# Performance work log

Measured on AMD Instinct MI355X. Metric: run time of the kernel, lower is better.

## Reference

```python
import jax, jax.numpy as jnp
import numpy as np

N_NODES = 50000
N_EDGES = 800000
D_IN = 16
H = 128
D_OUT = 8
N_LAYERS = 4


def _init_linear(key, fan_in, fan_out):
    # torch init: weight ~ N(0, 1/sqrt(in_features)), bias = 0
    W = jax.random.normal(key, (fan_in, fan_out), dtype=jnp.float32) / jnp.sqrt(jnp.float32(fan_in))
    b = jnp.zeros((fan_out,), dtype=jnp.float32)
    return W, b


def _mlp2(x, W1, b1, W2, b2):
    # 2-layer MLP: Linear -> GELU(exact) -> Linear
    h = jax.nn.gelu(x @ W1 + b1, approximate=False)
    return h @ W2 + b2


def setup_inputs() -> dict:
    key = jax.random.key(0)
    ks = jax.random.split(key, 16)
    node_features = jax.random.normal(ks[0], (N_NODES, D_IN), dtype=jnp.float32)
    edge_index = jax.random.randint(ks[1], (2, N_EDGES), 0, N_NODES, dtype=jnp.int64 if jax.config.jax_enable_x64 else jnp.int32)
    enc_W1, enc_b1 = _init_linear(ks[2], D_IN, H)
    enc_W2, enc_b2 = _init_linear(ks[3], H, H)
    dec_W1, dec_b1 = _init_linear(ks[4], H, H)
    dec_W2, dec_b2 = _init_linear(ks[5], H, D_OUT)
    # stacked per-layer params for the message-passing blocks
    eW1 = jnp.stack([_init_linear(jax.random.fold_in(ks[6], l), 2 * H, H)[0] for l in range(N_LAYERS)])
    eW2 = jnp.stack([_init_linear(jax.random.fold_in(ks[7], l), H, H)[0] for l in range(N_LAYERS)])
    nW1 = jnp.stack([_init_linear(jax.random.fold_in(ks[8], l), 2 * H, H)[0] for l in range(N_LAYERS)])
    nW2 = jnp.stack([_init_linear(jax.random.fold_in(ks[9], l), H, H)[0] for l in range(N_LAYERS)])
    eb1 = jnp.zeros((N_LAYERS, H), dtype=jnp.float32)
    eb2 = jnp.zeros((N_LAYERS, H), dtype=jnp.float32)
    nb1 = jnp.zeros((N_LAYERS, H), dtype=jnp.float32)
    nb2 = jnp.zeros((N_LAYERS, H), dtype=jnp.float32)
    return dict(node_features=node_features, edge_index=edge_index,
                enc_W1=enc_W1, enc_b1=enc_b1, enc_W2=enc_W2, enc_b2=enc_b2,
                edge_W1=eW1, edge_b1=eb1, edge_W2=eW2, edge_b2=eb2,
                node_W1=nW1, node_b1=nb1, node_W2=nW2, node_b2=nb2,
                dec_W1=dec_W1, dec_b1=dec_b1, dec_W2=dec_W2, dec_b2=dec_b2)


def reference(node_features, edge_index,
              enc_W1, enc_b1, enc_W2, enc_b2,
              edge_W1, edge_b1, edge_W2, edge_b2,
              node_W1, node_b1, node_W2, node_b2,
              dec_W1, dec_b1, dec_W2, dec_b2):
    src = edge_index[0]
    dst = edge_index[1]
    # encode
    h = _mlp2(node_features, enc_W1, enc_b1, enc_W2, enc_b2)  # [N, H]
    # process: residual message-passing blocks with sum aggregation
    for l in range(edge_W1.shape[0]):
        edge_input = jnp.concatenate([h[src], h[dst]], axis=-1)  # [E, 2H]
        message = _mlp2(edge_input, edge_W1[l], edge_b1[l], edge_W2[l], edge_b2[l])  # [E, H]
        aggregated = jax.ops.segment_sum(message, dst, num_segments=h.shape[0])  # [N, H]
        node_update = _mlp2(jnp.concatenate([h, aggregated], axis=-1),
                            node_W1[l], node_b1[l], node_W2[l], node_b2[l])
        h = h + node_update
    # decode
    return _mlp2(h, dec_W1, dec_b1, dec_W2, dec_b2)  # [N, D_OUT]
```

## Files before the change

kernel.cpp:

```cpp
#include <hip/hip_runtime.h>
#include <math.h>


constexpr int H = 128;
constexpr int NTHR = 256;
constexpr int TE = 64;
constexpr int TILE = 32;

using bf16x8 = __attribute__((ext_vector_type(8))) short;
using f32x4  = __attribute__((ext_vector_type(4))) float;

__device__ __forceinline__ float gelu_fast(float x) {
    const float u = fabsf(x) * 0.70710678118654752440f;
    const float t = __builtin_amdgcn_rcpf(fmaf(0.3275911f, u, 1.f));
    float p = fmaf(1.061405429f, t, -1.453152027f);
    p = fmaf(p, t, 1.421413741f);
    p = fmaf(p, t, -0.284496736f);
    p = fmaf(p, t, 0.254829592f);
    p = p * t;
    const float e = __expf(-u * u);
    float er = fmaf(-p, e, 1.f);
    er = copysignf(er, x);
    return 0.5f * x * (1.f + er);
}

__device__ __forceinline__ unsigned short f2bf(float f) {
    unsigned int u = __builtin_bit_cast(unsigned int, f);
    u = (u + 0x7fffu + ((u >> 16) & 1u)) >> 16;
    return (unsigned short)u;
}

__device__ __forceinline__ float bf2f_lo(unsigned int v) {
    return __builtin_bit_cast(float, v << 16);
}
__device__ __forceinline__ float bf2f_hi(unsigned int v) {
    return __builtin_bit_cast(float, v & 0xffff0000u);
}

__global__ __launch_bounds__(NTHR) void wcvt_kernel(
    const float* __restrict__ W, unsigned short* __restrict__ Wt,
    int K, int Ncols, int total) {
    const int i = blockIdx.x * NTHR + threadIdx.x;
    if (i >= total) return;
    const int per = K * Ncols;
    const int l = i / per;
    const int r = i - l * per;
    const int n = r % Ncols;
    const int k = r / Ncols;
    Wt[(size_t)l * per + n * K + k] = f2bf(W[i]);
}

__global__ __launch_bounds__(NTHR) void wcvt_top_kernel(
    const float* __restrict__ W, unsigned short* __restrict__ Wt, int total) {
    const int i = blockIdx.x * NTHR + threadIdx.x;
    if (i >= total) return;
    const int per = H * H;
    const int l = i / per;
    const int r = i - l * per;
    const int k = r / H;
    const int o = r % H;
    Wt[(size_t)l * H * 2 * H + o * 2 * H + k] =
        f2bf(W[(size_t)l * 2 * H * H + k * H + o]);
}

__global__ __launch_bounds__(H) void wcomb_kernel(
    const float* __restrict__ eW2, const float* __restrict__ eb2,
    const float* __restrict__ nW1, unsigned short* __restrict__ W1tc,
    float* __restrict__ cvec) {
    const int l = blockIdx.y;
    const int j = blockIdx.x;
    const int o = threadIdx.x;
    const float* w1 = nW1 + (size_t)l * 2 * H * H + (size_t)H * H;
    const float* row = (j < H) ? (eW2 + (size_t)l * H * H + (size_t)j * H)
                               : (eb2 + (size_t)l * H);
    float s = 0.f;
#pragma unroll 4
    for (int c = 0; c < H; ++c) s = fmaf(row[c], w1[(size_t)c * H + o], s);
    if (j < H)
        W1tc[(size_t)l * H * 2 * H + o * 2 * H + H + j] = f2bf(s);
    else
        cvec[(size_t)l * H + o] = s;
}

__global__ __launch_bounds__(NTHR) void deg_kernel(const int* __restrict__ dst,
                                                   int* __restrict__ deg, int E) {
    const int e = blockIdx.x * NTHR + threadIdx.x;
    if (e < E) atomicAdd(&deg[dst[e]], 1);
}

__global__ __launch_bounds__(1024) void scan1_kernel(
    const int* __restrict__ deg, int* __restrict__ out,
    int* __restrict__ bsum, int N) {
    __shared__ int buf[1024];
    const int t = threadIdx.x;
    const int i = blockIdx.x * 1024 + t;
    const int x = (i < N) ? deg[i] : 0;
    buf[t] = x;
    __syncthreads();
    int v = x;
    for (int off = 1; off < 1024; off <<= 1) {
        const int y = (t >= off) ? buf[t - off] : 0;
        __syncthreads();
        v += y;
        buf[t] = v;
        __syncthreads();
    }
    if (i < N) out[i] = v - x;
    if (t == 1023) bsum[blockIdx.x] = v;
}

__global__ void scan2_kernel(int* __restrict__ bsum, int nb) {
    if (threadIdx.x == 0) {
        int acc = 0;
        for (int i = 0; i < nb; ++i) {
            const int t = bsum[i];
            bsum[i] = acc;
            acc += t;
        }
    }
}

__global__ __launch_bounds__(NTHR) void scan3_kernel(
    int* __restrict__ out, int* __restrict__ cursor,
    const int* __restrict__ bsum, int N, int E) {
    const int i = blockIdx.x * NTHR + threadIdx.x;
    if (i < N) {
        const int v = out[i] + bsum[i >> 10];
        out[i] = v;
        cursor[i] = v;
    } else if (i == N) {
        out[N] = E;
    }
}

__global__ __launch_bounds__(NTHR) void chunk_kernel(
    const int* __restrict__ rowStart, int* __restrict__ chunkLo, int N) {
    const int n = blockIdx.x * NTHR + threadIdx.x;
    if (n < N) atomicMin(&chunkLo[rowStart[n] >> 5], n);
}

__global__ __launch_bounds__(NTHR) void scatter_kernel(
    const int* __restrict__ src, const int* __restrict__ dst,
    int* __restrict__ cursor, int* __restrict__ srcS, int E) {
    const int e = blockIdx.x * NTHR + threadIdx.x;
    if (e >= E) return;
    const int pos = atomicAdd(&cursor[dst[e]], 1);
    srcS[pos] = src[e];
}

__global__ __launch_bounds__(NTHR) void ab_kernel(
    const unsigned short* __restrict__ h_bf,
    const unsigned short* __restrict__ W1t,
    const float* __restrict__ b1, unsigned short* __restrict__ A,
    float* __restrict__ Bout, int N) {
    __shared__ __align__(16) unsigned short X[TE * H];
    const int t = threadIdx.x;
    const int lane = t & 63;
    const int w = t >> 6;
    const int n0 = blockIdx.x * TE;
    const int l15 = lane & 15;
    const int lq = lane >> 4;

#pragma unroll
    for (int i = 0; i < 4; ++i) {
        const int c = i * NTHR + t;
        const int row = c >> 4;
        const int col8 = c & 15;
        const int n = n0 + row;
        const int4 v = (n < N)
            ? *reinterpret_cast<const int4*>(h_bf + (size_t)n * H + col8 * 8)
            : make_int4(0, 0, 0, 0);
        const int byteoff = row * 256 + ((col8 * 16) ^ ((row & 7) << 4));
        *reinterpret_cast<int4*>(reinterpret_cast<char*>(X) + byteoff) = v;
    }

    const int half = w >> 1;
    const int cbase = (w & 1) * 64;
    bf16x8 Bf[4][4];
#pragma unroll
    for (int cg = 0; cg < 4; ++cg) {
        const int col = cbase + cg * 16 + l15;
#pragma unroll
        for (int s = 0; s < 4; ++s)
            Bf[cg][s] = *reinterpret_cast<const bf16x8*>(
                W1t + (size_t)col * 256 + half * 128 + s * 32 + lq * 8);
    }
    __syncthreads();

    f32x4 acc[4][4];
#pragma unroll
    for (int rg = 0; rg < 4; ++rg)
#pragma unroll
        for (int cg = 0; cg < 4; ++cg) acc[rg][cg] = (f32x4)0.f;

#pragma unroll
    for (int s = 0; s < 4; ++s) {
        bf16x8 a[4];
#pragma unroll
        for (int rg = 0; rg < 4; ++rg) {
            const int row = rg * 16 + l15;
            const int byteoff = row * 256 + ((s * 64 + lq * 16) ^ ((row & 7) << 4));
            a[rg] = *reinterpret_cast<const bf16x8*>(
                reinterpret_cast<const char*>(X) + byteoff);
        }
#pragma unroll
        for (int rg = 0; rg < 4; ++rg)
#pragma unroll
            for (int cg = 0; cg < 4; ++cg)
                acc[rg][cg] = __builtin_amdgcn_mfma_f32_16x16x32_bf16(
                    a[rg], Bf[cg][s], acc[rg][cg], 0, 0, 0);
    }

#pragma unroll
    for (int cg = 0; cg < 4; ++cg) {
        const int col = cbase + cg * 16 + l15;
        const float bb = (half == 1) ? b1[col] : 0.f;
#pragma unroll
        for (int rg = 0; rg < 4; ++rg) {
#pragma unroll
            for (int r = 0; r < 4; ++r) {
                const int row = rg * 16 + lq * 4 + r;
                const int n = n0 + row;
                if (n < N) {
                    if (half == 0)
                        A[(size_t)n * H + col] = f2bf(acc[rg][cg][r]);
                    else
                        Bout[(size_t)n * H + col] = acc[rg][cg][r] + bb;
                }
            }
        }
    }
}

__global__ __launch_bounds__(NTHR) void edge_gather_kernel(
    const unsigned short* __restrict__ A, const float* __restrict__ B,
    const int* __restrict__ srcS, const int* __restrict__ rowStart,
    const int* __restrict__ chunkLo, float* __restrict__ aggG, int N, int E) {
    const int lane = threadIdx.x & 63;
    const int c = blockIdx.x * 4 + (threadIdx.x >> 6);
    const int nWaves = (E >> 5) + 1;
    if (c >= nWaves) return;
    int n = chunkLo[c];
    if (n >= N) return;
    const int Wend = (c + 1) * 32;
    const int c2 = lane * 2;
    int r0 = rowStart[n];
    while (true) {
        const int r1 = rowStart[n + 1];
        const float2 bv = *reinterpret_cast<const float2*>(B + (size_t)n * H + c2);
        float s0 = 0.f, s1 = 0.f;
        int e = r0;
        for (; e + 4 <= r1; e += 4) {
            const int sa = srcS[e];
            const int sb = srcS[e + 1];
            const int sc = srcS[e + 2];
            const int sd = srcS[e + 3];
            const unsigned int va =
                *reinterpret_cast<const unsigned int*>(A + (size_t)sa * H + c2);
            const unsigned int vb =
                *reinterpret_cast<const unsigned int*>(A + (size_t)sb * H + c2);
            const unsigned int vc =
                *reinterpret_cast<const unsigned int*>(A + (size_t)sc * H + c2);
            const unsigned int vd =
                *reinterpret_cast<const unsigned int*>(A + (size_t)sd * H + c2);
            s0 += gelu_fast(bf2f_lo(va) + bv.x);
            s1 += gelu_fast(bf2f_hi(va) + bv.y);
            s0 += gelu_fast(bf2f_lo(vb) + bv.x);
            s1 += gelu_fast(bf2f_hi(vb) + bv.y);
            s0 += gelu_fast(bf2f_lo(vc) + bv.x);
            s1 += gelu_fast(bf2f_hi(vc) + bv.y);
            s0 += gelu_fast(bf2f_lo(vd) + bv.x);
            s1 += gelu_fast(bf2f_hi(vd) + bv.y);
        }
        for (; e < r1; ++e) {
            const int s = srcS[e];
            const unsigned int av =
                *reinterpret_cast<const unsigned int*>(A + (size_t)s * H + c2);
            s0 += gelu_fast(bf2f_lo(av) + bv.x);
            s1 += gelu_fast(bf2f_hi(av) + bv.y);
        }
        *reinterpret_cast<float2*>(aggG + (size_t)n * H + c2) =
            make_float2(s0, s1);
        if (++n >= N) break;
        r0 = r1;
        if (r0 >= Wend) break;
    }
}

template <bool PROD>
__global__ __launch_bounds__(NTHR) void node_fused_kernel(
    float* __restrict__ h, unsigned short* __restrict__ h_bf,
    const float* __restrict__ aggG, const int* __restrict__ deg,
    const unsigned short* __restrict__ W1tc, const float* __restrict__ b1,
    const float* __restrict__ cvec, const unsigned short* __restrict__ W2t,
    const float* __restrict__ b2, const unsigned short* __restrict__ eW1tN,
    const float* __restrict__ eb1N, unsigned short* __restrict__ A_out,
    float* __restrict__ B_out, int N) {
    __shared__ __align__(16) unsigned short X[TE * 256];
    __shared__ int degS[TE];
    const int t = threadIdx.x;
    const int lane = t & 63;
    const int w = t >> 6;
    const int n0 = blockIdx.x * TE;
    const int l15 = lane & 15;
    const int lq = lane >> 4;

    if (t < TE) degS[t] = (n0 + t < N) ? deg[n0 + t] : 0;
#pragma unroll
    for (int i = 0; i < 8; ++i) {
        const int c = i * NTHR + t;
        const int row = c >> 5;
        const int col8 = c & 31;
        const int n = n0 + row;
        int4 v = make_int4(0, 0, 0, 0);
        if (n < N) {
            if (col8 < 16) {
                v = *reinterpret_cast<const int4*>(h_bf + (size_t)n * H + col8 * 8);
            } else {
                const float* ap = aggG + (size_t)n * H + (col8 - 16) * 8;
                union { int4 q; unsigned short us[8]; } u;
#pragma unroll
                for (int j = 0; j < 8; ++j) u.us[j] = f2bf(ap[j]);
                v = u.q;
            }
        }
        const int byteoff = row * 512 + ((col8 * 16) ^ ((row & 7) << 4));
        *reinterpret_cast<int4*>(reinterpret_cast<char*>(X) + byteoff) = v;
    }

    bf16x8 B1[2][8];
#pragma unroll
    for (int cg = 0; cg < 2; ++cg) {
        const int col = w * 32 + cg * 16 + l15;
#pragma unroll
        for (int s = 0; s < 8; ++s)
            B1[cg][s] = *reinterpret_cast<const bf16x8*>(
                W1tc + (size_t)col * 256 + s * 32 + lq * 8);
    }
    __syncthreads();

    f32x4 acc[4][2];
#pragma unroll
    for (int rg = 0; rg < 4; ++rg)
#pragma unroll
        for (int cg = 0; cg < 2; ++cg) acc[rg][cg] = (f32x4)0.f;

#pragma unroll
    for (int s = 0; s < 8; ++s) {
        bf16x8 a[4];
#pragma unroll
        for (int rg = 0; rg < 4; ++rg) {
            const int row = rg * 16 + l15;
            const int byteoff = row * 512 + ((s * 64 + lq * 16) ^ ((row & 7) << 4));
            a[rg] = *reinterpret_cast<const bf16x8*>(
                reinterpret_cast<const char*>(X) + byteoff);
        }
#pragma unroll
        for (int rg = 0; rg < 4; ++rg)
#pragma unroll
            for (int cg = 0; cg < 2; ++cg)
                acc[rg][cg] = __builtin_amdgcn_mfma_f32_16x16x32_bf16(
                    a[rg], B1[cg][s], acc[rg][cg], 0, 0, 0);
    }
    __syncthreads();

#pragma unroll
    for (int cg = 0; cg < 2; ++cg) {
        const int col = w * 32 + cg * 16 + l15;
        const float bb = b1[col];
        const float cc = cvec[col];
#pragma unroll
        for (int rg = 0; rg < 4; ++rg) {
#pragma unroll
            for (int r = 0; r < 4; ++r) {
                const int row = rg * 16 + lq * 4 + r;
                const float v =
                    gelu_fast(acc[rg][cg][r] + bb + (float)degS[row] * cc);
                const int byteoff = row * 256 + ((col * 2) ^ ((row & 7) << 4));
                *reinterpret_cast<unsigned short*>(
                    reinterpret_cast<char*>(X) + byteoff) = f2bf(v);
            }
        }
    }

    bf16x8 B2[2][4];
#pragma unroll
    for (int cg = 0; cg < 2; ++cg) {
        const int col = w * 32 + cg * 16 + l15;
#pragma unroll
        for (int s = 0; s < 4; ++s)
            B2[cg][s] = *reinterpret_cast<const bf16x8*>(
                W2t + (size_t)col * 128 + s * 32 + lq * 8);
    }
    __syncthreads();

    f32x4 acc2[4][2];
#pragma unroll
    for (int rg = 0; rg < 4; ++rg)
#pragma unroll
        for (int cg = 0; cg < 2; ++cg) acc2[rg][cg] = (f32x4)0.f;

#pragma unroll
    for (int s = 0; s < 4; ++s) {
        bf16x8 a[4];
#pragma unroll
        for (int rg = 0; rg < 4; ++rg) {
            const int row = rg * 16 + l15;
            const int byteoff = row * 256 + ((s * 64 + lq * 16) ^ ((row & 7) << 4));
            a[rg] = *reinterpret_cast<const bf16x8*>(
                reinterpret_cast<const char*>(X) + byteoff);
        }
#pragma unroll
        for (int rg = 0; rg < 4; ++rg)
#pragma unroll
            for (int cg = 0; cg < 2; ++cg)
                acc2[rg][cg] = __builtin_amdgcn_mfma_f32_16x16x32_bf16(
                    a[rg], B2[cg][s], acc2[rg][cg], 0, 0, 0);
    }

#pragma unroll
    for (int cg = 0; cg < 2; ++cg) {
        const int col = w * 32 + cg * 16 + l15;
        const float bb = b2[col];
#pragma unroll
        for (int rg = 0; rg < 4; ++rg) {
#pragma unroll
            for (int r = 0; r < 4; ++r) {
                const int row = rg * 16 + lq * 4 + r;
                const int n = n0 + row;
                if (n < N) {
                    const float hv = h[(size_t)n * H + col] + acc2[rg][cg][r] + bb;
                    h[(size_t)n * H + col] = hv;
                    const unsigned short hb = f2bf(hv);
                    h_bf[(size_t)n * H + col] = hb;
                    if (PROD) {
                        const int byteoff =
                            16384 + row * 256 + ((col * 2) ^ ((row & 7) << 4));
                        *reinterpret_cast<unsigned short*>(
                            reinterpret_cast<char*>(X) + byteoff) = hb;
                    }
                } else if (PROD) {
                    const int byteoff =
                        16384 + row * 256 + ((col * 2) ^ ((row & 7) << 4));
                    *reinterpret_cast<unsigned short*>(
                        reinterpret_cast<char*>(X) + byteoff) = 0;
                }
            }
        }
    }

    if (PROD) {
        bf16x8 B3[2][4], B4[2][4];
#pragma unroll
        for (int cg = 0; cg < 2; ++cg) {
            const int col = w * 32 + cg * 16 + l15;
#pragma unroll
            for (int s = 0; s < 4; ++s) {
                B3[cg][s] = *reinterpret_cast<const bf16x8*>(
                    eW1tN + (size_t)col * 256 + s * 32 + lq * 8);
                B4[cg][s] = *reinterpret_cast<const bf16x8*>(
                    eW1tN + (size_t)col * 256 + 128 + s * 32 + lq * 8);
            }
        }
        __syncthreads();

        f32x4 acc3[4][2], acc4[4][2];
#pragma unroll
        for (int rg = 0; rg < 4; ++rg)
#pragma unroll
            for (int cg = 0; cg < 2; ++cg) {
                acc3[rg][cg] = (f32x4)0.f;
                acc4[rg][cg] = (f32x4)0.f;
            }

#pragma unroll
        for (int s = 0; s < 4; ++s) {
            bf16x8 a[4];
#pragma unroll
            for (int rg = 0; rg < 4; ++rg) {
                const int row = rg * 16 + l15;
                const int byteoff =
                    16384 + row * 256 + ((s * 64 + lq * 16) ^ ((row & 7) << 4));
                a[rg] = *reinterpret_cast<const bf16x8*>(
                    reinterpret_cast<const char*>(X) + byteoff);
            }
#pragma unroll
            for (int rg = 0; rg < 4; ++rg)
#pragma unroll
                for (int cg = 0; cg < 2; ++cg) {
                    acc3[rg][cg] = __builtin_amdgcn_mfma_f32_16x16x32_bf16(
                        a[rg], B3[cg][s], acc3[rg][cg], 0, 0, 0);
                    acc4[rg][cg] = __builtin_amdgcn_mfma_f32_16x16x32_bf16(
                        a[rg], B4[cg][s], acc4[rg][cg], 0, 0, 0);
                }
        }

#pragma unroll
        for (int cg = 0; cg < 2; ++cg) {
            const int col = w * 32 + cg * 16 + l15;
            const float bb = eb1N[col];
#pragma unroll
            for (int rg = 0; rg < 4; ++rg) {
#pragma unroll
                for (int r = 0; r < 4; ++r) {
                    const int row = rg * 16 + lq * 4 + r;
                    const int n = n0 + row;
                    if (n < N) {
                        A_out[(size_t)n * H + col] = f2bf(acc3[rg][cg][r]);
                        B_out[(size_t)n * H + col] = acc4[rg][cg][r] + bb;
                    }
                }
            }
        }
    }
}

template <int K4>
__device__ __forceinline__ void mlp_layer(const float* __restrict__ W,
                                          const float* lds, int ldsStride,
                                          int c0, int egBase,
                                          float a0[8], float a1[8]) {
#pragma unroll 2
    for (int k4 = 0; k4 < K4; ++k4) {
        const float w00 = W[(k4 * 4 + 0) * H + c0];
        const float w01 = W[(k4 * 4 + 1) * H + c0];
        const float w02 = W[(k4 * 4 + 2) * H + c0];
        const float w03 = W[(k4 * 4 + 3) * H + c0];
        const float w10 = W[(k4 * 4 + 0) * H + c0 + 64];
        const float w11 = W[(k4 * 4 + 1) * H + c0 + 64];
        const float w12 = W[(k4 * 4 + 2) * H + c0 + 64];
        const float w13 = W[(k4 * 4 + 3) * H + c0 + 64];
#pragma unroll
        for (int e = 0; e < 8; ++e) {
            const float4 x = *reinterpret_cast<const float4*>(
                &lds[(egBase + e) * ldsStride + k4 * 4]);
            a0[e] = fmaf(x.x, w00, a0[e]);
            a0[e] = fmaf(x.y, w01, a0[e]);
            a0[e] = fmaf(x.z, w02, a0[e]);
            a0[e] = fmaf(x.w, w03, a0[e]);
            a1[e] = fmaf(x.x, w10, a1[e]);
            a1[e] = fmaf(x.y, w11, a1[e]);
            a1[e] = fmaf(x.z, w12, a1[e]);
            a1[e] = fmaf(x.w, w13, a1[e]);
        }
    }
}

__global__ __launch_bounds__(NTHR) void encode_kernel(
    const float* __restrict__ nf, const float* __restrict__ W1,
    const float* __restrict__ b1, const float* __restrict__ W2,
    const float* __restrict__ b2, float* __restrict__ h,
    unsigned short* __restrict__ h_bf, int N) {
    __shared__ float xin[TILE * 16];
    __shared__ float hm[TILE * H];
    const int t = threadIdx.x;
    const int n0 = blockIdx.x * TILE;
    const int c0 = t & 63;
    const int eg = t >> 6;

    for (int i = t; i < TILE * 16; i += NTHR) {
        const int gi = n0 * 16 + i;
        xin[i] = (gi < N * 16) ? nf[gi] : 0.f;
    }
    __syncthreads();

    float a0[8], a1[8];
#pragma unroll
    for (int e = 0; e < 8; ++e) { a0[e] = 0.f; a1[e] = 0.f; }
    mlp_layer<4>(W1, xin, 16, c0, eg * 8, a0, a1);
    {
        const float bb0 = b1[c0], bb1 = b1[c0 + 64];
#pragma unroll
        for (int e = 0; e < 8; ++e) {
            hm[(eg * 8 + e) * H + c0] = gelu_fast(a0[e] + bb0);
            hm[(eg * 8 + e) * H + c0 + 64] = gelu_fast(a1[e] + bb1);
        }
    }
    __syncthreads();
#pragma unroll
    for (int e = 0; e < 8; ++e) { a0[e] = 0.f; a1[e] = 0.f; }
    mlp_layer<32>(W2, hm, H, c0, eg * 8, a0, a1);
    const float bb0 = b2[c0], bb1 = b2[c0 + 64];
#pragma unroll
    for (int e = 0; e < 8; ++e) {
        const int n = n0 + eg * 8 + e;
        if (n < N) {
            const float v0 = a0[e] + bb0, v1 = a1[e] + bb1;
            h[(size_t)n * H + c0] = v0;
            h[(size_t)n * H + c0 + 64] = v1;
            h_bf[(size_t)n * H + c0] = f2bf(v0);
            h_bf[(size_t)n * H + c0 + 64] = f2bf(v1);
        }
    }
}

__global__ __launch_bounds__(NTHR) void decode_kernel(
    const float* __restrict__ h, const float* __restrict__ W1,
    const float* __restrict__ b1, const float* __restrict__ W2,
    const float* __restrict__ b2, float* __restrict__ out, int N) {
    __shared__ float xin[TILE * H];
    __shared__ float hm[TILE * 132];
    const int t = threadIdx.x;
    const int n0 = blockIdx.x * TILE;
    const int c0 = t & 63;
    const int eg = t >> 6;
    {
        const int col = t & 127;
        for (int e = t >> 7; e < TILE; e += 2) {
            const int n = n0 + e;
            xin[e * H + col] = (n < N) ? h[(size_t)n * H + col] : 0.f;
        }
    }
    __syncthreads();

    float a0[8], a1[8];
#pragma unroll
    for (int e = 0; e < 8; ++e) { a0[e] = 0.f; a1[e] = 0.f; }
    mlp_layer<32>(W1, xin, H, c0, eg * 8, a0, a1);
    {
        const float bb0 = b1[c0], bb1 = b1[c0 + 64];
#pragma unroll
        for (int e = 0; e < 8; ++e) {
            hm[(eg * 8 + e) * 132 + c0] = gelu_fast(a0[e] + bb0);
            hm[(eg * 8 + e) * 132 + c0 + 64] = gelu_fast(a1[e] + bb1);
        }
    }
    __syncthreads();
    {
        const int e = t >> 3;
        const int o = t & 7;
        const int n = n0 + e;
        float acc = b2[o];
#pragma unroll 4
        for (int k = 0; k < H; ++k)
            acc = fmaf(hm[e * 132 + k], W2[k * 8 + o], acc);
        if (n < N) out[n * 8 + o] = acc;
    }
}

extern "C" void kernel_launch(void* const* d_in, const int* in_sizes, int n_in,
                              void* d_out, int out_size, void* d_ws,
                              size_t ws_size, hipStream_t stream) {
    (void)n_in; (void)out_size; (void)ws_size;
    const float* nf      = (const float*)d_in[0];
    const int*   ei      = (const int*)d_in[1];
    const float* enc_W1  = (const float*)d_in[2];
    const float* enc_b1  = (const float*)d_in[3];
    const float* enc_W2  = (const float*)d_in[4];
    const float* enc_b2  = (const float*)d_in[5];
    const float* edge_W1 = (const float*)d_in[6];
    const float* edge_b1 = (const float*)d_in[7];
    const float* edge_W2 = (const float*)d_in[8];
    const float* edge_b2 = (const float*)d_in[9];
    const float* node_W1 = (const float*)d_in[10];
    const float* node_b1 = (const float*)d_in[11];
    const float* node_W2 = (const float*)d_in[12];
    const float* node_b2 = (const float*)d_in[13];
    const float* dec_W1  = (const float*)d_in[14];
    const float* dec_b1  = (const float*)d_in[15];
    const float* dec_W2  = (const float*)d_in[16];
    const float* dec_b2  = (const float*)d_in[17];

    const int N = in_sizes[0] / 16;
    const int E = in_sizes[1] / 2;
    const int L = in_sizes[7] / H;
    const int numChunks = (E >> 5) + 1;

    char* ws = (char*)d_ws;
    float* h    = (float*)ws;                    ws += (size_t)N * H * 4;
    float* aggG = (float*)ws;                    ws += (size_t)N * H * 4;
    float* Bf32 = (float*)ws;                    ws += (size_t)N * H * 4;
    unsigned short* h_bf  = (unsigned short*)ws; ws += (size_t)N * H * 2;
    unsigned short* A_bf  = (unsigned short*)ws; ws += (size_t)N * H * 2;
    int* srcS     = (int*)ws;                    ws += (size_t)E * 4;
    int* deg      = (int*)ws;                    ws += (size_t)N * 4;
    int* rowStart = (int*)ws;                    ws += (size_t)(N + 1) * 4;
    int* cursor   = (int*)ws;                    ws += (size_t)N * 4;
    int* bsum     = (int*)ws;                    ws += (size_t)256 * 4;
    int* chunkLo  = (int*)ws;                    ws += (size_t)numChunks * 4;
    unsigned short* eW1t = (unsigned short*)ws;  ws += (size_t)L * 2 * H * H * 2;
    unsigned short* nW1tc = (unsigned short*)ws; ws += (size_t)L * 2 * H * H * 2;
    unsigned short* nW2t = (unsigned short*)ws;  ws += (size_t)L * H * H * 2;
    float* cvec   = (float*)ws;                  ws += (size_t)L * H * 4;

    const int* srcArr = ei;
    const int* dstArr = ei + E;

    {
        const int t1 = L * 2 * H * H, t2 = L * H * H;
        wcvt_kernel<<<(t1 + NTHR - 1) / NTHR, NTHR, 0, stream>>>(edge_W1, eW1t, 2 * H, H, t1);
        wcvt_kernel<<<(t2 + NTHR - 1) / NTHR, NTHR, 0, stream>>>(node_W2, nW2t, H, H, t2);
        wcvt_top_kernel<<<(t2 + NTHR - 1) / NTHR, NTHR, 0, stream>>>(node_W1, nW1tc, t2);
        wcomb_kernel<<<dim3(H + 1, L), H, 0, stream>>>(edge_W2, edge_b2,
                                                       node_W1, nW1tc, cvec);
    }

    hipMemsetAsync(deg, 0, (size_t)N * 4, stream);
    deg_kernel<<<(E + NTHR - 1) / NTHR, NTHR, 0, stream>>>(dstArr, deg, E);
    const int nScanB = (N + 1023) / 1024;
    scan1_kernel<<<nScanB, 1024, 0, stream>>>(deg, rowStart, bsum, N);
    scan2_kernel<<<1, 64, 0, stream>>>(bsum, nScanB);
    scan3_kernel<<<(N + 1 + NTHR - 1) / NTHR, NTHR, 0, stream>>>(
        rowStart, cursor, bsum, N, E);
    hipMemsetAsync(chunkLo, 0x7f, (size_t)numChunks * 4, stream);
    chunk_kernel<<<(N + NTHR - 1) / NTHR, NTHR, 0, stream>>>(rowStart, chunkLo, N);
    scatter_kernel<<<(E + NTHR - 1) / NTHR, NTHR, 0, stream>>>(srcArr, dstArr,
                                                               cursor, srcS, E);

    const int encBlocks  = (N + TILE - 1) / TILE;
    const int tileBlocks = (N + TE - 1) / TE;
    const int gatherBlks = (numChunks + 3) / 4;

    encode_kernel<<<encBlocks, NTHR, 0, stream>>>(nf, enc_W1, enc_b1, enc_W2,
                                                  enc_b2, h, h_bf, N);
    ab_kernel<<<tileBlocks, NTHR, 0, stream>>>(h_bf, eW1t, edge_b1, A_bf, Bf32,
                                               N);
    for (int l = 0; l < L; ++l) {
        edge_gather_kernel<<<gatherBlks, NTHR, 0, stream>>>(
            A_bf, Bf32, srcS, rowStart, chunkLo, aggG, N, E);
        if (l + 1 < L) {
            node_fused_kernel<true><<<tileBlocks, NTHR, 0, stream>>>(
                h, h_bf, aggG, deg, nW1tc + (size_t)l * 2 * H * H,
                node_b1 + (size_t)l * H, cvec + (size_t)l * H,
                nW2t + (size_t)l * H * H, node_b2 + (size_t)l * H,
                eW1t + (size_t)(l + 1) * 2 * H * H,
                edge_b1 + (size_t)(l + 1) * H, A_bf, Bf32, N);
        } else {
            node_fused_kernel<false><<<tileBlocks, NTHR, 0, stream>>>(
                h, h_bf, aggG, deg, nW1tc + (size_t)l * 2 * H * H,
                node_b1 + (size_t)l * H, cvec + (size_t)l * H,
                nW2t + (size_t)l * H * H, node_b2 + (size_t)l * H, nullptr,
                nullptr, nullptr, nullptr, N);
        }
    }
    decode_kernel<<<encBlocks, NTHR, 0, stream>>>(h, dec_W1, dec_b1, dec_W2,
                                                  dec_b2, (float*)d_out, N);
}
```

Measured before the change: 719.0 us.

## Fuse edge gather-aggregation into node kernel with double-buffered A/B

Moves the per-destination edge gather, GELU and sum directly into the node MLP kernel. Each wave aggregates 16 node rows and writes the bf16 result straight into shared memory, which removes the separate gather kernel, the fp32 aggregation buffer round-trip, and the chunk-map setup. A and B are double-buffered so the next layer's projections can be written while the current ones are still being read. Source indices are pre-scaled by 256 bytes to simplify addressing, and the three weight-conversion kernels are merged into one launch. The cost is that per-tile gather work is now uneven, with a full tile of row aggregation serialized across only 4 waves before the MFMA work begins.

```diff
diff --git a/kernel.cpp b/kernel.cpp
--- a/kernel.cpp
+++ b/kernel.cpp
@@ -37,30 +37,37 @@
     return __builtin_bit_cast(float, v & 0xffff0000u);
 }
 
-__global__ __launch_bounds__(NTHR) void wcvt_kernel(
-    const float* __restrict__ W, unsigned short* __restrict__ Wt,
-    int K, int Ncols, int total) {
+__global__ __launch_bounds__(NTHR) void prep_kernel(
+    const float* __restrict__ eW1, const float* __restrict__ nW2,
+    const float* __restrict__ nW1, unsigned short* __restrict__ eW1t,
+    unsigned short* __restrict__ nW2t, unsigned short* __restrict__ nW1tc,
+    int t1, int t2) {
     const int i = blockIdx.x * NTHR + threadIdx.x;
-    if (i >= total) return;
-    const int per = K * Ncols;
-    const int l = i / per;
-    const int r = i - l * per;
-    const int n = r % Ncols;
-    const int k = r / Ncols;
-    Wt[(size_t)l * per + n * K + k] = f2bf(W[i]);
-}
-
-__global__ __launch_bounds__(NTHR) void wcvt_top_kernel(
-    const float* __restrict__ W, unsigned short* __restrict__ Wt, int total) {
-    const int i = blockIdx.x * NTHR + threadIdx.x;
-    if (i >= total) return;
-    const int per = H * H;
-    const int l = i / per;
-    const int r = i - l * per;
-    const int k = r / H;
-    const int o = r % H;
-    Wt[(size_t)l * H * 2 * H + o * 2 * H + k] =
-        f2bf(W[(size_t)l * 2 * H * H + k * H + o]);
+    if (i < t1) {
+        const int per = 2 * H * H;
+        const int l = i / per;
+        const int r = i - l * per;
+        const int n = r % H;
+        const int k = r / H;
+        eW1t[(size_t)l * per + n * 2 * H + k] = f2bf(eW1[i]);
+    } else if (i < t1 + t2) {
+        const int j = i - t1;
+        const int per = H * H;
+        const int l = j / per;
+        const int r = j - l * per;
+        const int n = r % H;
+        const int k = r / H;
+        nW2t[(size_t)l * per + n * H + k] = f2bf(nW2[j]);
+    } else if (i < t1 + 2 * t2) {
+        const int j = i - t1 - t2;
+        const int per = H * H;
+        const int l = j / per;
+        const int r = j - l * per;
+        const int k = r / H;
+        const int o = r % H;
+        nW1tc[(size_t)l * H * 2 * H + o * 2 * H + k] =
+            f2bf(nW1[(size_t)l * 2 * H * H + k * H + o]);
+    }
 }
 
 __global__ __launch_bounds__(H) void wcomb_kernel(
@@ -133,19 +140,13 @@
     }
 }
 
-__global__ __launch_bounds__(NTHR) void chunk_kernel(
-    const int* __restrict__ rowStart, int* __restrict__ chunkLo, int N) {
-    const int n = blockIdx.x * NTHR + threadIdx.x;
-    if (n < N) atomicMin(&chunkLo[rowStart[n] >> 5], n);
-}
-
 __global__ __launch_bounds__(NTHR) void scatter_kernel(
     const int* __restrict__ src, const int* __restrict__ dst,
     int* __restrict__ cursor, int* __restrict__ srcS, int E) {
     const int e = blockIdx.x * NTHR + threadIdx.x;
     if (e >= E) return;
     const int pos = atomicAdd(&cursor[dst[e]], 1);
-    srcS[pos] = src[e];
+    srcS[pos] = src[e] << 8;
 }
 
 __global__ __launch_bounds__(NTHR) void ab_kernel(
@@ -232,70 +233,16 @@
     }
 }
 
-__global__ __launch_bounds__(NTHR) void edge_gather_kernel(
-    const unsigned short* __restrict__ A, const float* __restrict__ B,
-    const int* __restrict__ srcS, const int* __restrict__ rowStart,
-    const int* __restrict__ chunkLo, float* __restrict__ aggG, int N, int E) {
-    const int lane = threadIdx.x & 63;
-    const int c = blockIdx.x * 4 + (threadIdx.x >> 6);
-    const int nWaves = (E >> 5) + 1;
-    if (c >= nWaves) return;
-    int n = chunkLo[c];
-    if (n >= N) return;
-    const int Wend = (c + 1) * 32;
-    const int c2 = lane * 2;
-    int r0 = rowStart[n];
-    while (true) {
-        const int r1 = rowStart[n + 1];
-        const float2 bv = *reinterpret_cast<const float2*>(B + (size_t)n * H + c2);
-        float s0 = 0.f, s1 = 0.f;
-        int e = r0;
-        for (; e + 4 <= r1; e += 4) {
-            const int sa = srcS[e];
-            const int sb = srcS[e + 1];
-            const int sc = srcS[e + 2];
-            const int sd = srcS[e + 3];
-            const unsigned int va =
-                *reinterpret_cast<const unsigned int*>(A + (size_t)sa * H + c2);
-            const unsigned int vb =
-                *reinterpret_cast<const unsigned int*>(A + (size_t)sb * H + c2);
-            const unsigned int vc =
-                *reinterpret_cast<const unsigned int*>(A + (size_t)sc * H + c2);
-            const unsigned int vd =
-                *reinterpret_cast<const unsigned int*>(A + (size_t)sd * H + c2);
-            s0 += gelu_fast(bf2f_lo(va) + bv.x);
-            s1 += gelu_fast(bf2f_hi(va) + bv.y);
-            s0 += gelu_fast(bf2f_lo(vb) + bv.x);
-            s1 += gelu_fast(bf2f_hi(vb) + bv.y);
-            s0 += gelu_fast(bf2f_lo(vc) + bv.x);
-            s1 += gelu_fast(bf2f_hi(vc) + bv.y);
-            s0 += gelu_fast(bf2f_lo(vd) + bv.x);
-            s1 += gelu_fast(bf2f_hi(vd) + bv.y);
-        }
-        for (; e < r1; ++e) {
-            const int s = srcS[e];
-            const unsigned int av =
-                *reinterpret_cast<const unsigned int*>(A + (size_t)s * H + c2);
-            s0 += gelu_fast(bf2f_lo(av) + bv.x);
-            s1 += gelu_fast(bf2f_hi(av) + bv.y);
-        }
-        *reinterpret_cast<float2*>(aggG + (size_t)n * H + c2) =
-            make_float2(s0, s1);
-        if (++n >= N) break;
-        r0 = r1;
-        if (r0 >= Wend) break;
-    }
-}
-
 template <bool PROD>
 __global__ __launch_bounds__(NTHR) void node_fused_kernel(
     float* __restrict__ h, unsigned short* __restrict__ h_bf,
-    const float* __restrict__ aggG, const int* __restrict__ deg,
-    const unsigned short* __restrict__ W1tc, const float* __restrict__ b1,
-    const float* __restrict__ cvec, const unsigned short* __restrict__ W2t,
-    const float* __restrict__ b2, const unsigned short* __restrict__ eW1tN,
-    const float* __restrict__ eb1N, unsigned short* __restrict__ A_out,
-    float* __restrict__ B_out, int N) {
+    const unsigned short* __restrict__ A_g, const float* __restrict__ B_g,
+    const int* __restrict__ srcS, const int* __restrict__ rowStart,
+    const int* __restrict__ deg, const unsigned short* __restrict__ W1tc,
+    const float* __restrict__ b1, const float* __restrict__ cvec,
+    const unsigned short* __restrict__ W2t, const float* __restrict__ b2,
+    const unsigned short* __restrict__ eW1tN, const float* __restrict__ eb1N,
+    unsigned short* __restrict__ A_out, float* __restrict__ B_out, int N) {
     __shared__ __align__(16) unsigned short X[TE * 256];
     __shared__ int degS[TE];
     const int t = threadIdx.x;
@@ -306,26 +253,68 @@
     const int lq = lane >> 4;
 
     if (t < TE) degS[t] = (n0 + t < N) ? deg[n0 + t] : 0;
-#pragma unroll
-    for (int i = 0; i < 8; ++i) {
+
+#pragma unroll
+    for (int i = 0; i < 4; ++i) {
         const int c = i * NTHR + t;
-        const int row = c >> 5;
-        const int col8 = c & 31;
+        const int row = c >> 4;
+        const int col8 = c & 15;
         const int n = n0 + row;
-        int4 v = make_int4(0, 0, 0, 0);
-        if (n < N) {
-            if (col8 < 16) {
-                v = *reinterpret_cast<const int4*>(h_bf + (size_t)n * H + col8 * 8);
-            } else {
-                const float* ap = aggG + (size_t)n * H + (col8 - 16) * 8;
-                union { int4 q; unsigned short us[8]; } u;
-#pragma unroll
-                for (int j = 0; j < 8; ++j) u.us[j] = f2bf(ap[j]);
-                v = u.q;
-            }
-        }
+        const int4 v = (n < N)
+            ? *reinterpret_cast<const int4*>(h_bf + (size_t)n * H + col8 * 8)
+            : make_int4(0, 0, 0, 0);
         const int byteoff = row * 512 + ((col8 * 16) ^ ((row & 7) << 4));
         *reinterpret_cast<int4*>(reinterpret_cast<char*>(X) + byteoff) = v;
+    }
+
+    {
+        const char* Abase = (const char*)A_g + (size_t)(lane * 4);
+        const int c2 = lane * 2;
+        for (int rr = 0; rr < 16; ++rr) {
+            const int row = w * 16 + rr;
+            const int n = n0 + row;
+            float s0 = 0.f, s1 = 0.f;
+            if (n < N) {
+                const int r0 = rowStart[n];
+                const int r1 = rowStart[n + 1];
+                const float2 bv =
+                    *reinterpret_cast<const float2*>(B_g + (size_t)n * H + c2);
+                int e = r0;
+                for (; e + 4 <= r1; e += 4) {
+                    const int sa = srcS[e];
+                    const int sb = srcS[e + 1];
+                    const int sc = srcS[e + 2];
+                    const int sd = srcS[e + 3];
+                    const unsigned int va =
+                        *reinterpret_cast<const unsigned int*>(Abase + sa);
+                    const unsigned int vb =
+                        *reinterpret_cast<const unsigned int*>(Abase + sb);
+                    const unsigned int vc =
+                        *reinterpret_cast<const unsigned int*>(Abase + sc);
+                    const unsigned int vd =
+                        *reinterpret_cast<const unsigned int*>(Abase + sd);
+                    s0 += gelu_fast(bf2f_lo(va) + bv.x);
+                    s1 += gelu_fast(bf2f_hi(va) + bv.y);
+                    s0 += gelu_fast(bf2f_lo(vb) + bv.x);
+                    s1 += gelu_fast(bf2f_hi(vb) + bv.y);
+                    s0 += gelu_fast(bf2f_lo(vc) + bv.x);
+                    s1 += gelu_fast(bf2f_hi(vc) + bv.y);
+                    s0 += gelu_fast(bf2f_lo(vd) + bv.x);
+                    s1 += gelu_fast(bf2f_hi(vd) + bv.y);
+                }
+                for (; e < r1; ++e) {
+                    const unsigned int av =
+                        *reinterpret_cast<const unsigned int*>(Abase + srcS[e]);
+                    s0 += gelu_fast(bf2f_lo(av) + bv.x);
+                    s1 += gelu_fast(bf2f_hi(av) + bv.y);
+                }
+            }
+            const unsigned int packed =
+                (unsigned int)f2bf(s0) | ((unsigned int)f2bf(s1) << 16);
+            const int byteoff = row * 512 + ((256 + lane * 4) ^ ((row & 7) << 4));
+            *reinterpret_cast<unsigned int*>(reinterpret_cast<char*>(X) +
+                                             byteoff) = packed;
+        }
     }
 
     bf16x8 B1[2][8];
@@ -664,20 +653,21 @@
     const int N = in_sizes[0] / 16;
     const int E = in_sizes[1] / 2;
     const int L = in_sizes[7] / H;
-    const int numChunks = (E >> 5) + 1;
 
     char* ws = (char*)d_ws;
     float* h    = (float*)ws;                    ws += (size_t)N * H * 4;
-    float* aggG = (float*)ws;                    ws += (size_t)N * H * 4;
-    float* Bf32 = (float*)ws;                    ws += (size_t)N * H * 4;
-    unsigned short* h_bf  = (unsigned short*)ws; ws += (size_t)N * H * 2;
-    unsigned short* A_bf  = (unsigned short*)ws; ws += (size_t)N * H * 2;
+    float* Bbuf[2];
+    Bbuf[0] = (float*)ws;                        ws += (size_t)N * H * 4;
+    Bbuf[1] = (float*)ws;                        ws += (size_t)N * H * 4;
+    unsigned short* h_bf = (unsigned short*)ws;  ws += (size_t)N * H * 2;
+    unsigned short* Abuf[2];
+    Abuf[0] = (unsigned short*)ws;               ws += (size_t)N * H * 2;
+    Abuf[1] = (unsigned short*)ws;               ws += (size_t)N * H * 2;
     int* srcS     = (int*)ws;                    ws += (size_t)E * 4;
     int* deg      = (int*)ws;                    ws += (size_t)N * 4;
     int* rowStart = (int*)ws;                    ws += (size_t)(N + 1) * 4;
     int* cursor   = (int*)ws;                    ws += (size_t)N * 4;
     int* bsum     = (int*)ws;                    ws += (size_t)256 * 4;
-    int* chunkLo  = (int*)ws;                    ws += (size_t)numChunks * 4;
     unsigned short* eW1t = (unsigned short*)ws;  ws += (size_t)L * 2 * H * H * 2;
     unsigned short* nW1tc = (unsigned short*)ws; ws += (size_t)L * 2 * H * H * 2;
     unsigned short* nW2t = (unsigned short*)ws;  ws += (size_t)L * H * H * 2;
@@ -688,9 +678,8 @@
 
     {
         const int t1 = L * 2 * H * H, t2 = L * H * H;
-        wcvt_kernel<<<(t1 + NTHR - 1) / NTHR, NTHR, 0, stream>>>(edge_W1, eW1t, 2 * H, H, t1);
-        wcvt_kernel<<<(t2 + NTHR - 1) / NTHR, NTHR, 0, stream>>>(node_W2, nW2t, H, H, t2);
-        wcvt_top_kernel<<<(t2 + NTHR - 1) / NTHR, NTHR, 0, stream>>>(node_W1, nW1tc, t2);
+        prep_kernel<<<(t1 + 2 * t2 + NTHR - 1) / NTHR, NTHR, 0, stream>>>(
+            edge_W1, node_W2, node_W1, eW1t, nW2t, nW1tc, t1, t2);
         wcomb_kernel<<<dim3(H + 1, L), H, 0, stream>>>(edge_W2, edge_b2,
                                                        node_W1, nW1tc, cvec);
     }
@@ -702,35 +691,31 @@
     scan2_kernel<<<1, 64, 0, stream>>>(bsum, nScanB);
     scan3_kernel<<<(N + 1 + NTHR - 1) / NTHR, NTHR, 0, stream>>>(
         rowStart, cursor, bsum, N, E);
-    hipMemsetAsync(chunkLo, 0x7f, (size_t)numChunks * 4, stream);
-    chunk_kernel<<<(N + NTHR - 1) / NTHR, NTHR, 0, stream>>>(rowStart, chunkLo, N);
     scatter_kernel<<<(E + NTHR - 1) / NTHR, NTHR, 0, stream>>>(srcArr, dstArr,
                                                                cursor, srcS, E);
 
     const int encBlocks  = (N + TILE - 1) / TILE;
     const int tileBlocks = (N + TE - 1) / TE;
-    const int gatherBlks = (numChunks + 3) / 4;
 
     encode_kernel<<<encBlocks, NTHR, 0, stream>>>(nf, enc_W1, enc_b1, enc_W2,
                                                   enc_b2, h, h_bf, N);
-    ab_kernel<<<tileBlocks, NTHR, 0, stream>>>(h_bf, eW1t, edge_b1, A_bf, Bf32,
-                                               N);
+    ab_kernel<<<tileBlocks, NTHR, 0, stream>>>(h_bf, eW1t, edge_b1, Abuf[0],
+                                               Bbuf[0], N);
     for (int l = 0; l < L; ++l) {
-        edge_gather_kernel<<<gatherBlks, NTHR, 0, stream>>>(
-            A_bf, Bf32, srcS, rowStart, chunkLo, aggG, N, E);
+        const int cur = l & 1;
         if (l + 1 < L) {
             node_fused_kernel<true><<<tileBlocks, NTHR, 0, stream>>>(
-                h, h_bf, aggG, deg, nW1tc + (size_t)l * 2 * H * H,
-                node_b1 + (size_t)l * H, cvec + (size_t)l * H,
-                nW2t + (size_t)l * H * H, node_b2 + (size_t)l * H,
-                eW1t + (size_t)(l + 1) * 2 * H * H,
-                edge_b1 + (size_t)(l + 1) * H, A_bf, Bf32, N);
+                h, h_bf, Abuf[cur], Bbuf[cur], srcS, rowStart, deg,
+                nW1tc + (size_t)l * 2 * H * H, node_b1 + (size_t)l * H,
+                cvec + (size_t)l * H, nW2t + (size_t)l * H * H,
+                node_b2 + (size_t)l * H, eW1t + (size_t)(l + 1) * 2 * H * H,
+                edge_b1 + (size_t)(l + 1) * H, Abuf[cur ^ 1], Bbuf[cur ^ 1], N);
         } else {
             node_fused_kernel<false><<<tileBlocks, NTHR, 0, stream>>>(
-                h, h_bf, aggG, deg, nW1tc + (size_t)l * 2 * H * H,
-                node_b1 + (size_t)l * H, cvec + (size_t)l * H,
-                nW2t + (size_t)l * H * H, node_b2 + (size_t)l * H, nullptr,
-                nullptr, nullptr, nullptr, N);
+                h, h_bf, Abuf[cur], Bbuf[cur], srcS, rowStart, deg,
+                nW1tc + (size_t)l * 2 * H * H, node_b1 + (size_t)l * H,
+                cvec + (size_t)l * H, nW2t + (size_t)l * H * H,
+                node_b2 + (size_t)l * H, nullptr, nullptr, nullptr, nullptr, N);
         }
     }
     decode_kernel<<<encBlocks, NTHR, 0, stream>>>(h, dec_W1, dec_b1, dec_W2,
```

Measured after the change: 966.6 us. 34.4% more time.
